# Optimization experiments

Measured on AMD Instinct MI355X. Metric: run time of the kernel, lower is better.

The kernel has to match this reference:

```python
import jax, jax.numpy as jnp
import numpy as np

N_HEADS = 16
KEY_DIM = 64
VAL_DIM = 64
HIDDEN = 1024
SCALE = 1.0 / float(KEY_DIM) ** 0.5


def setup_inputs() -> dict:
    key = jax.random.key(0)
    ks = jax.random.split(key, 16)
    B, Lq, Lk, R = 2, 2048, 2048, 2048
    inp = {
        "query": jax.random.normal(ks[0], (B, Lq, HIDDEN), jnp.float32),
        "value": jax.random.normal(ks[1], (B, Lk, HIDDEN), jnp.float32),
        "positional_embedding": jax.random.normal(ks[2], (R, HIDDEN), jnp.float32),
        "u_weight": jax.random.normal(ks[3], (N_HEADS, KEY_DIM), jnp.float32) * 0.02,
        "v_weight": jax.random.normal(ks[4], (N_HEADS, KEY_DIM), jnp.float32) * 0.02,
        "indices": jax.random.randint(ks[5], (2, Lq, Lk), 0, R, jnp.int64 if jax.config.jax_enable_x64 else jnp.int32),
        "lower": jax.random.uniform(ks[6], (Lq, Lk), jnp.float32),
    }
    s = 0.02
    inp["Wq"] = jax.random.normal(ks[7], (HIDDEN, N_HEADS * KEY_DIM), jnp.float32) * s
    inp["bq"] = jnp.zeros((N_HEADS * KEY_DIM,), jnp.float32)
    inp["Wk"] = jax.random.normal(ks[8], (HIDDEN, N_HEADS * KEY_DIM), jnp.float32) * s
    inp["bk"] = jnp.zeros((N_HEADS * KEY_DIM,), jnp.float32)
    inp["Wv"] = jax.random.normal(ks[9], (HIDDEN, N_HEADS * VAL_DIM), jnp.float32) * s
    inp["bv"] = jnp.zeros((N_HEADS * VAL_DIM,), jnp.float32)
    inp["Wr"] = jax.random.normal(ks[10], (HIDDEN, N_HEADS * KEY_DIM), jnp.float32) * s
    inp["br"] = jnp.zeros((N_HEADS * KEY_DIM,), jnp.float32)
    inp["Wo"] = jax.random.normal(ks[11], (N_HEADS * VAL_DIM, HIDDEN), jnp.float32) * s
    inp["bo"] = jnp.zeros((HIDDEN,), jnp.float32)
    return inp


def reference(query, value, positional_embedding, u_weight, v_weight, indices, lower,
              Wq, bq, Wk, bk, Wv, bv, Wr, br, Wo, bo):
    B, Lq, _ = query.shape
    Lk = value.shape[1]
    R = positional_embedding.shape[0]
    # projections (torch Linear with weights stored as [in, out])
    q = (query @ Wq + bq).reshape(B, Lq, N_HEADS, KEY_DIM)
    k = (value @ Wk + bk).reshape(B, Lk, N_HEADS, KEY_DIM)
    v = (value @ Wv + bv).reshape(B, Lk, N_HEADS, VAL_DIM)
    r = (positional_embedding @ Wr + br).reshape(R, N_HEADS, KEY_DIM)
    # content (AC) and position (BD) score terms -> [i, j, b, n]
    AC = jnp.einsum("bind,bjnd->ijbn", q + u_weight, k)
    BD = jnp.einsum("bind,jnd->ijbn", q + v_weight, r)
    # rel-shift: gather [Lq, R] -> [Lq, Lk] positions, then apply lower mask
    BD = BD[indices[0], indices[1]] * lower[:, :, None, None]
    attn = jax.nn.softmax((AC + BD) * SCALE, axis=1)  # softmax over key dim j
    out = jnp.einsum("ijbn,bjnd->bind", attn, v).reshape(B, Lq, N_HEADS * VAL_DIM)
    return out @ Wo + bo
```

## Files before the change

### kernel.cpp

```cpp
#include <hip/hip_runtime.h>
#include <stdint.h>

typedef __attribute__((ext_vector_type(8))) short short8;
typedef __attribute__((ext_vector_type(4))) float f32x4;
typedef unsigned short u16;
typedef unsigned int u32;
typedef unsigned long long u64;

#define LQ 2048
#define LK 2048
#define RDIM 2048
#define HID 1024
#define NH 16
#define DH 64
#define S2SCALE 0.1803368801111204f

__device__ __forceinline__ float bf2f(u16 u){
  union { unsigned int i; float f; } v; v.i = ((unsigned int)u) << 16; return v.f;
}
__device__ __forceinline__ u16 f2bf(float f){
  union { float f; unsigned int i; } v; v.f = f;
  unsigned int r = v.i + 0x7fffu + ((v.i >> 16) & 1u);
  return (u16)(r >> 16);
}
__device__ __forceinline__ f32x4 fzero(){ f32x4 z = {0.0f, 0.0f, 0.0f, 0.0f}; return z; }

__global__ void k_detect(const u32* __restrict__ q, const u32* __restrict__ idxw,
                         int* __restrict__ flags){
  int t = threadIdx.x;
  u32 w = q[t];
  int b = (w >> 7) & 0xFF;
  unsigned long long mb = __ballot(b >= 100 && b <= 140);
  u32 hi = idxw[2 * t + 1];
  unsigned long long mi = __ballot(hi == 0u);
  if (t == 0){
    flags[0] = (__popcll(mb) >= 48) ? 1 : 0;
    flags[1] = (__popcll(mi) == 64) ? 1 : 0;
  }
}

struct Seg { const void* src; u16* dst; int n4; };
struct SegPack { Seg s[8]; };
__global__ void k_ingestN(SegPack p, const int* __restrict__ flags){
  int f = flags[0];
  Seg sg = p.s[blockIdx.y];
  int stride = gridDim.x * blockDim.x;
  for (int i = blockIdx.x * blockDim.x + threadIdx.x; i < sg.n4; i += stride){
    if (f){
      reinterpret_cast<uint2*>(sg.dst)[i] = reinterpret_cast<const uint2*>(sg.src)[i];
    } else {
      float4 v = reinterpret_cast<const float4*>(sg.src)[i];
      union { u16 h[4]; uint2 u; } t;
      t.h[0] = f2bf(v.x); t.h[1] = f2bf(v.y); t.h[2] = f2bf(v.z); t.h[3] = f2bf(v.w);
      reinterpret_cast<uint2*>(sg.dst)[i] = t.u;
    }
  }
}

struct WPack { const void* src[5]; u16* dst[5]; };
__global__ void k_wtrans(WPack p, const int* __restrict__ flags){
  int f = flags[0];
  const void* W = p.src[blockIdx.z];
  u16* Wt = p.dst[blockIdx.z];
  __shared__ u16 t[64][65];
  int tid = threadIdx.x;
  int bx = blockIdx.x, by = blockIdx.y;
#pragma unroll
  for (int it = 0; it < 16; ++it){
    int id = it * 256 + tid;
    int r = id >> 6, c = id & 63;
    size_t so = (size_t)(by * 64 + r) * HID + bx * 64 + c;
    t[r][c] = f ? ((const u16*)W)[so] : f2bf(((const float*)W)[so]);
  }
  __syncthreads();
#pragma unroll
  for (int it = 0; it < 16; ++it){
    int id = it * 256 + tid;
    int r = id >> 6, c = id & 63;
    Wt[(size_t)(bx * 64 + r) * HID + by * 64 + c] = t[c][r];
  }
}

__global__ void k_goff(const int* __restrict__ idx, int* __restrict__ goff,
                       const int* __restrict__ flags){
  int i64f = flags[1];
  const size_t N = (size_t)LQ * LK;
  size_t stride = (size_t)gridDim.x * blockDim.x;
  for (size_t t = (size_t)blockIdx.x * blockDim.x + threadIdx.x; t < N; t += stride){
    long long a0, a1;
    if (i64f){
      const long long* ip = (const long long*)idx;
      a0 = ip[t]; a1 = ip[N + t];
    } else {
      a0 = idx[t]; a1 = idx[N + t];
    }
    goff[t] = (int)(a0 * RDIM + a1);
  }
}

__global__ void k_gemm(const u16* __restrict__ A, const u16* __restrict__ Bt,
                       const u16* __restrict__ bias,
                       const u16* __restrict__ add0, const u16* __restrict__ add1,
                       void* __restrict__ D0, u16* __restrict__ D1,
                       int headmajor, const int* __restrict__ oflags){
  __shared__ u16 As[128][72];
  __shared__ u16 Bs[128][72];
  int tid = threadIdx.x;
  int l = tid & 63, w = tid >> 6;
  int lr = l & 15, g = l >> 4;
  int wr = w >> 1, wc = w & 1;
  int outf32 = oflags ? (oflags[0] == 0) : 0;
  f32x4 acc[4][4];
#pragma unroll
  for (int a = 0; a < 4; ++a)
#pragma unroll
    for (int bq_ = 0; bq_ < 4; ++bq_) acc[a][bq_] = fzero();
  const size_t arowg = (size_t)blockIdx.x * 128;
  const size_t browg = (size_t)blockIdx.y * 128;
  for (int kt = 0; kt < HID; kt += 64){
#pragma unroll
    for (int it = 0; it < 4; ++it){
      int id = it * 256 + tid;
      int r = id >> 3, ch = id & 7;
      uint4 va = *reinterpret_cast<const uint4*>(A + (arowg + r) * HID + kt + ch * 8);
      *reinterpret_cast<uint4*>(&As[r][ch * 8]) = va;
      uint4 vb = *reinterpret_cast<const uint4*>(Bt + (browg + r) * HID + kt + ch * 8);
      *reinterpret_cast<uint4*>(&Bs[r][ch * 8]) = vb;
    }
    __syncthreads();
#pragma unroll
    for (int ks = 0; ks < 2; ++ks){
      short8 af[4], bfv[4];
#pragma unroll
      for (int mf = 0; mf < 4; ++mf)
        af[mf] = *reinterpret_cast<const short8*>(&As[wr * 64 + mf * 16 + lr][ks * 32 + 8 * g]);
#pragma unroll
      for (int nf = 0; nf < 4; ++nf)
        bfv[nf] = *reinterpret_cast<const short8*>(&Bs[wc * 64 + nf * 16 + lr][ks * 32 + 8 * g]);
#pragma unroll
      for (int mf = 0; mf < 4; ++mf)
#pragma unroll
        for (int nf = 0; nf < 4; ++nf)
          acc[mf][nf] = __builtin_amdgcn_mfma_f32_16x16x32_bf16(af[mf], bfv[nf], acc[mf][nf], 0, 0, 0);
    }
    __syncthreads();
  }
#pragma unroll
  for (int mf = 0; mf < 4; ++mf)
#pragma unroll
    for (int nf = 0; nf < 4; ++nf){
      int col = (int)browg + wc * 64 + nf * 16 + lr;
      float bcol = bf2f(bias[col]);
      float a0 = add0 ? bf2f(add0[col]) : 0.0f;
      float a1 = add1 ? bf2f(add1[col]) : 0.0f;
#pragma unroll
      for (int reg = 0; reg < 4; ++reg){
        int row = (int)arowg + wr * 64 + mf * 16 + 4 * g + reg;
        float base = acc[mf][nf][reg] + bcol;
        if (headmajor == 2){
          int b = row >> 11, i = row & 2047;
          int n32 = col >> 6, d = col & 63;
          u16* Dx = (n32 < NH) ? (u16*)D0 : D1;
          size_t dst = ((size_t)(b * NH + (n32 & (NH - 1))) * LQ + i) * DH + d;
          Dx[dst] = f2bf(base);
        } else if (headmajor == 1){
          int b = row >> 11, i = row & 2047;
          int n = col >> 6, d = col & 63;
          size_t dst = ((size_t)(b * NH + n) * LQ + i) * DH + d;
          ((u16*)D0)[dst] = f2bf(base + a0);
          if (D1) D1[dst] = f2bf(base + a1);
        } else {
          size_t dst = (size_t)row * HID + col;
          if (outf32) ((float*)D0)[dst] = base;
          else        ((u16*)D0)[dst] = f2bf(base);
        }
      }
    }
}

__global__ void k_bdfull16(const u16* __restrict__ qv, const u16* __restrict__ rr,
                           u16* __restrict__ bdf, int bnBase){
  __shared__ u16 tile[32][64][16];
  int tid = threadIdx.x;
  int l = tid & 63, w = tid >> 6;
  int lr = l & 15, g = l >> 4;
  int i0 = blockIdx.x * 32, j0 = blockIdx.y * 64;
#pragma unroll
  for (int hh = 0; hh < 4; ++hh){
    int g_ = w * 4 + hh;
    int bn = bnBase + g_;
    int b = bn >> 4, n = bn & 15;
    const u16* qb = qv + ((size_t)(b * NH + n) * LQ + i0) * DH;
    const u16* rb = rr + ((size_t)n * RDIM + j0) * DH;
    short8 af[2][2];
#pragma unroll
    for (int mf = 0; mf < 2; ++mf)
#pragma unroll
      for (int ks = 0; ks < 2; ++ks)
        af[mf][ks] = *reinterpret_cast<const short8*>(qb + (size_t)(mf * 16 + lr) * DH + ks * 32 + 8 * g);
    f32x4 acc[2][4];
#pragma unroll
    for (int mf = 0; mf < 2; ++mf)
#pragma unroll
      for (int nf = 0; nf < 4; ++nf) acc[mf][nf] = fzero();
#pragma unroll
    for (int nf = 0; nf < 4; ++nf){
#pragma unroll
      for (int ks = 0; ks < 2; ++ks){
        short8 bb = *reinterpret_cast<const short8*>(rb + (size_t)(nf * 16 + lr) * DH + ks * 32 + 8 * g);
#pragma unroll
        for (int mf = 0; mf < 2; ++mf)
          acc[mf][nf] = __builtin_amdgcn_mfma_f32_16x16x32_bf16(af[mf][ks], bb, acc[mf][nf], 0, 0, 0);
      }
    }
#pragma unroll
    for (int mf = 0; mf < 2; ++mf)
#pragma unroll
      for (int nf = 0; nf < 4; ++nf)
#pragma unroll
        for (int reg = 0; reg < 4; ++reg)
          tile[mf * 16 + 4 * g + reg][nf * 16 + lr][g_] = f2bf(acc[mf][nf][reg]);
  }
  __syncthreads();
#pragma unroll
  for (int e = 0; e < 32; ++e){
    int id = e * 256 + tid;
    int line = id >> 2, part = id & 3;
    int ii = line >> 6, jj = line & 63;
    u64 v = *reinterpret_cast<const u64*>(&tile[ii][jj][part * 4]);
    *reinterpret_cast<u64*>(
        bdf + ((size_t)(i0 + ii) * RDIM + (size_t)(j0 + jj)) * 16 + part * 4) = v;
  }
}

template<int G>
__global__ void k_bdfull(const u16* __restrict__ qv, const u16* __restrict__ rr,
                         u16* __restrict__ bdf, int bnBase){
  __shared__ u16 tile[16][32][G];
  int tid = threadIdx.x;
  int l = tid & 63, w = tid >> 6;
  int lr = l & 15, g = l >> 4;
  int i0 = blockIdx.x * 16, j0 = blockIdx.y * 32;
  constexpr int C = (G >= 4) ? (G / 4) : 1;
  if (G >= 4 || w < G){
#pragma unroll
    for (int bi = 0; bi < C; ++bi){
      int g_ = w * C + bi;
      int bn = bnBase + g_;
      int b = bn >> 4, n = bn & 15;
      const u16* qb = qv + ((size_t)(b * NH + n) * LQ + i0) * DH;
      const u16* rb = rr + ((size_t)n * RDIM + j0) * DH;
      f32x4 acc2[2];
      acc2[0] = fzero(); acc2[1] = fzero();
#pragma unroll
      for (int ks = 0; ks < 2; ++ks){
        short8 a = *reinterpret_cast<const short8*>(qb + (size_t)lr * DH + ks * 32 + 8 * g);
#pragma unroll
        for (int nf = 0; nf < 2; ++nf){
          short8 bb = *reinterpret_cast<const short8*>(rb + (size_t)(lr + 16 * nf) * DH + ks * 32 + 8 * g);
          acc2[nf] = __builtin_amdgcn_mfma_f32_16x16x32_bf16(a, bb, acc2[nf], 0, 0, 0);
        }
      }
#pragma unroll
      for (int nf = 0; nf < 2; ++nf){
        int jj = lr + 16 * nf;
#pragma unroll
        for (int reg = 0; reg < 4; ++reg)
          tile[4 * g + reg][jj][g_] = f2bf(acc2[nf][reg]);
      }
    }
  }
  __syncthreads();
  constexpr int W = (G >= 4) ? 4 : G;
  constexpr int PARTS = G / W;
  constexpr int CHUNKS = 512 * PARTS;
#pragma unroll
  for (int e = 0; e < (CHUNKS + 255) / 256; ++e){
    int id = e * 256 + tid;
    if (CHUNKS < 256 * ((CHUNKS + 255) / 256) && id >= CHUNKS) break;
    int line = id / PARTS, part = id % PARTS;
    int ii = line >> 5, jj = line & 31;
    int k = part * W;
    const u16* src = &tile[ii][jj][k];
    u16* dst = bdf + ((size_t)(i0 + ii) * RDIM + (size_t)(j0 + jj)) * G + k;
    if (W == 4)
      *reinterpret_cast<u64*>(dst) = *reinterpret_cast<const u64*>(src);
    else if (W == 2)
      *reinterpret_cast<u32*>(dst) = *reinterpret_cast<const u32*>(src);
    else
      *dst = *src;
  }
}

template<int G>
__global__ void k_gather(const u16* __restrict__ bdf, const int* __restrict__ goff,
                         const u16* __restrict__ lower, u16* __restrict__ bdg){
  __shared__ u16 tile[G][16][32];
  int tid = threadIdx.x;
  int i0 = blockIdx.x * 16, j0 = blockIdx.y * 32;
#pragma unroll
  for (int it = 0; it < 2; ++it){
    int p = it * 256 + tid;
    int ii = p >> 5, jj = p & 31;
    size_t off = (size_t)(i0 + ii) * LK + (j0 + jj);
    int go = goff[off];
    float lw = bf2f(lower[off]);
    const u16* src = bdf + (size_t)go * G;
    union { uint4 q[2]; u32 w2[8]; u16 h[16]; } uv;
    if (G == 16){
      uv.q[0] = *reinterpret_cast<const uint4*>(src);
      uv.q[1] = *reinterpret_cast<const uint4*>(src + 8);
    } else if (G == 8){
      uv.q[0] = *reinterpret_cast<const uint4*>(src);
    } else if (G == 2){
      uv.w2[0] = *reinterpret_cast<const u32*>(src);
    } else {
      uv.h[0] = *src;
    }
#pragma unroll
    for (int k = 0; k < G; ++k)
      tile[k][ii][jj] = f2bf(bf2f(uv.h[k]) * lw);
  }
  __syncthreads();
  constexpr int CHUNKS = G * 128;
#pragma unroll
  for (int e = 0; e < (CHUNKS + 255) / 256; ++e){
    int id = e * 256 + tid;
    if (CHUNKS < 256 * ((CHUNKS + 255) / 256) && id >= CHUNKS) break;
    int g_ = id >> 7, rem = id & 127;
    int ii = rem >> 3, part = rem & 7;
    u64 v = *reinterpret_cast<const u64*>(&tile[g_][ii][part * 4]);
    *reinterpret_cast<u64*>(
        bdg + (size_t)g_ * LQ * LK + (size_t)(i0 + ii) * LK + j0 + part * 4) = v;
  }
}

__global__ void k_flash(const u16* __restrict__ qu, const u16* __restrict__ kk,
                        const u16* __restrict__ vv, const u16* __restrict__ bdg,
                        u16* __restrict__ oo, int bnBase){
  __shared__ u16 klds[128][72];
  __shared__ u16 vtlds[64][136];
  __shared__ u16 plds[4][16][136];
  int tid = threadIdx.x;
  int l = tid & 63, w = tid >> 6;
  int lr = l & 15, g = l >> 4;
  int gi = blockIdx.x;
  int bn = bnBase + gi;
  int b = bn >> 4, n = bn & 15;
  int i0 = blockIdx.y * 64;
  const u16* qb = qu + ((size_t)bn * LQ + i0 + w * 16) * DH;
  short8 aq0 = *reinterpret_cast<const short8*>(qb + (size_t)lr * DH + 8 * g);
  short8 aq1 = *reinterpret_cast<const short8*>(qb + (size_t)lr * DH + 32 + 8 * g);
  f32x4 O[4];
#pragma unroll
  for (int nf = 0; nf < 4; ++nf) O[nf] = fzero();
  float mrun[4], lacc[4];
#pragma unroll
  for (int r = 0; r < 4; ++r){ mrun[r] = -1e30f; lacc[r] = 0.0f; }
  const u16* kbase = kk + (size_t)bn * LK * DH;
  const u16* vbase = vv + (size_t)bn * LK * DH;
  const u16* bdb = bdg + (size_t)gi * LQ * LK + (size_t)(i0 + w * 16) * LK;

  for (int j0 = 0; j0 < LK; j0 += 128){
#pragma unroll
    for (int it = 0; it < 4; ++it){
      int id = it * 256 + tid;
      int r = id >> 3, ch = id & 7;
      uint4 kv = *reinterpret_cast<const uint4*>(kbase + (size_t)(j0 + r) * DH + ch * 8);
      *reinterpret_cast<uint4*>(&klds[r][ch * 8]) = kv;
      uint4 vv4 = *reinterpret_cast<const uint4*>(vbase + (size_t)(j0 + r) * DH + ch * 8);
      u16 tmp[8];
      *reinterpret_cast<uint4*>(tmp) = vv4;
#pragma unroll
      for (int e2 = 0; e2 < 8; ++e2) vtlds[ch * 8 + e2][r] = tmp[e2];
    }
    __syncthreads();

    float sv[8][4];
#pragma unroll
    for (int nf = 0; nf < 8; ++nf){
      f32x4 z = fzero();
      short8 bk0 = *reinterpret_cast<const short8*>(&klds[lr + 16 * nf][8 * g]);
      short8 bk1 = *reinterpret_cast<const short8*>(&klds[lr + 16 * nf][32 + 8 * g]);
      z = __builtin_amdgcn_mfma_f32_16x16x32_bf16(aq0, bk0, z, 0, 0, 0);
      z = __builtin_amdgcn_mfma_f32_16x16x32_bf16(aq1, bk1, z, 0, 0, 0);
#pragma unroll
      for (int reg = 0; reg < 4; ++reg){
        float bd = bf2f(bdb[(size_t)(4 * g + reg) * LK + j0 + lr + 16 * nf]);
        sv[nf][reg] = (z[reg] + bd) * S2SCALE;
      }
    }
    float fs[4];
#pragma unroll
    for (int reg = 0; reg < 4; ++reg){
      float mx = sv[0][reg];
#pragma unroll
      for (int nf = 1; nf < 8; ++nf) mx = fmaxf(mx, sv[nf][reg]);
#pragma unroll
      for (int d = 1; d < 16; d <<= 1) mx = fmaxf(mx, __shfl_xor(mx, d));
      float mnew = fmaxf(mrun[reg], mx);
      fs[reg] = exp2f(mrun[reg] - mnew);
      mrun[reg] = mnew;
      float sumloc = 0.0f;
#pragma unroll
      for (int nf = 0; nf < 8; ++nf){
        sv[nf][reg] = exp2f(sv[nf][reg] - mnew);
        sumloc += sv[nf][reg];
      }
      lacc[reg] = lacc[reg] * fs[reg] + sumloc;
    }
#pragma unroll
    for (int nf = 0; nf < 4; ++nf)
#pragma unroll
      for (int reg = 0; reg < 4; ++reg)
        O[nf][reg] *= fs[reg];
#pragma unroll
    for (int nf = 0; nf < 8; ++nf)
#pragma unroll
      for (int reg = 0; reg < 4; ++reg)
        plds[w][4 * g + reg][lr + 16 * nf] = f2bf(sv[nf][reg]);
    short8 pa[4];
#pragma unroll
    for (int ks = 0; ks < 4; ++ks)
      pa[ks] = *reinterpret_cast<const short8*>(&plds[w][lr][ks * 32 + 8 * g]);
#pragma unroll
    for (int nf = 0; nf < 4; ++nf){
#pragma unroll
      for (int ks = 0; ks < 4; ++ks){
        short8 bv = *reinterpret_cast<const short8*>(&vtlds[lr + 16 * nf][ks * 32 + 8 * g]);
        O[nf] = __builtin_amdgcn_mfma_f32_16x16x32_bf16(pa[ks], bv, O[nf], 0, 0, 0);
      }
    }
    __syncthreads();
  }
  float lsum[4];
#pragma unroll
  for (int reg = 0; reg < 4; ++reg){
    float s = lacc[reg];
#pragma unroll
    for (int d = 1; d < 16; d <<= 1) s += __shfl_xor(s, d);
    lsum[reg] = s;
  }
#pragma unroll
  for (int nf = 0; nf < 4; ++nf)
#pragma unroll
    for (int reg = 0; reg < 4; ++reg){
      int i = i0 + w * 16 + 4 * g + reg;
      float vo = O[nf][reg] / lsum[reg];
      oo[((size_t)(b * LQ + i)) * HID + n * DH + lr + 16 * nf] = f2bf(vo);
    }
}

extern "C" void kernel_launch(void* const* d_in, const int* in_sizes, int n_in,
                              void* d_out, int out_size, void* d_ws, size_t ws_size,
                              hipStream_t stream){
  const void* query = d_in[0];
  const void* value = d_in[1];
  const void* pos   = d_in[2];
  const void* uw    = d_in[3];
  const void* vw    = d_in[4];
  const int* idx    = (const int*)d_in[5];
  const void* lower = d_in[6];
  const void* Wq = d_in[7];  const void* bq = d_in[8];
  const void* Wk = d_in[9];  const void* bk = d_in[10];
  const void* Wv = d_in[11]; const void* bv = d_in[12];
  const void* Wr = d_in[13]; const void* br = d_in[14];
  const void* Wo = d_in[15]; const void* bo = d_in[16];
  (void)in_sizes; (void)n_in; (void)out_size;

  char* ws = (char*)d_ws;
  const size_t MB = (size_t)1 << 20;
  u16* cquery = (u16*)(ws + 0 * MB);
  u16* cvalue = (u16*)(ws + 8 * MB);
  int* goff   = (int*)(ws + 0 * MB);
  u16* cpos   = (u16*)(ws + 16 * MB);
  u16* clower = (u16*)(ws + 20 * MB);
  char* sm = ws + 38 * MB;
  u16* cuw = (u16*)(sm + 0 * 4096);
  u16* cvw = (u16*)(sm + 1 * 4096);
  u16* cbq = (u16*)(sm + 2 * 4096);
  u16* cbk = (u16*)(sm + 3 * 4096);
  u16* cbv = cbk + 1024;
  u16* cbr = (u16*)(sm + 5 * 4096);
  u16* cbo = (u16*)(sm + 6 * 4096);
  int* flags = (int*)(sm + 7 * 4096);
  u16* wqt = (u16*)(ws + 39 * MB);
  u16* wkt = (u16*)(ws + 41 * MB);
  u16* wvt = (u16*)(ws + 43 * MB);
  u16* wrt = (u16*)(ws + 45 * MB);
  u16* wot = (u16*)(ws + 47 * MB);
  u16* qu  = (u16*)(ws + 49 * MB);
  u16* qv  = (u16*)(ws + 57 * MB);
  u16* kkp = (u16*)(ws + 65 * MB);
  u16* vvp = (u16*)(ws + 73 * MB);
  u16* rrp = (u16*)(ws + 81 * MB);
  u16* oo  = (u16*)(ws + 85 * MB);
  u16* bdf = (u16*)(ws + 96 * MB);

  int G = 1;
  if (ws_size >= 352 * MB) G = 16;
  else if (ws_size >= 224 * MB) G = 8;
  else if (ws_size >= 128 * MB) G = 2;
  u16* bdg = (u16*)(ws + (96 + 8 * (size_t)G) * MB);

  dim3 blk(256);
  k_detect<<<1, 64, 0, stream>>>((const u32*)query, (const u32*)idx, flags);

  {
    SegPack big;
    big.s[0] = { query, cquery, 2 * LQ * HID / 4 };
    big.s[1] = { value, cvalue, 2 * LK * HID / 4 };
    big.s[2] = { pos,   cpos,   RDIM * HID / 4 };
    big.s[3] = { lower, clower, LQ * LK / 4 };
    for (int i = 4; i < 8; ++i) big.s[i] = { nullptr, nullptr, 0 };
    k_ingestN<<<dim3(512, 4), blk, 0, stream>>>(big, flags);
    SegPack sml;
    sml.s[0] = { uw, cuw, NH * DH / 4 };
    sml.s[1] = { vw, cvw, NH * DH / 4 };
    sml.s[2] = { bq, cbq, HID / 4 };
    sml.s[3] = { bk, cbk, HID / 4 };
    sml.s[4] = { bv, cbv, HID / 4 };
    sml.s[5] = { br, cbr, HID / 4 };
    sml.s[6] = { bo, cbo, HID / 4 };
    sml.s[7] = { nullptr, nullptr, 0 };
    k_ingestN<<<dim3(4, 7), blk, 0, stream>>>(sml, flags);
  }
  {
    WPack wp;
    wp.src[0] = Wq; wp.dst[0] = wqt;
    wp.src[1] = Wk; wp.dst[1] = wkt;
    wp.src[2] = Wv; wp.dst[2] = wvt;
    wp.src[3] = Wr; wp.dst[3] = wrt;
    wp.src[4] = Wo; wp.dst[4] = wot;
    k_wtrans<<<dim3(16, 16, 5), blk, 0, stream>>>(wp, flags);
  }

  k_gemm<<<dim3(32, 8), blk, 0, stream>>>(cquery, wqt, cbq, cuw, cvw, qu, qv, 1, nullptr);
  k_gemm<<<dim3(32, 16), blk, 0, stream>>>(cvalue, wkt, cbk, nullptr, nullptr, kkp, vvp, 2, nullptr);
  k_gemm<<<dim3(16, 8), blk, 0, stream>>>(cpos, wrt, cbr, nullptr, nullptr, rrp, nullptr, 1, nullptr);

  k_goff<<<dim3(1024), blk, 0, stream>>>(idx, goff, flags);

  for (int b0 = 0; b0 < 2 * NH; b0 += G){
    if (G == 16){
      k_bdfull16<<<dim3(64, 32), blk, 0, stream>>>(qv, rrp, bdf, b0);
      k_gather<16><<<dim3(128, 64), blk, 0, stream>>>(bdf, goff, clower, bdg);
    } else if (G == 8){
      k_bdfull<8><<<dim3(128, 64), blk, 0, stream>>>(qv, rrp, bdf, b0);
      k_gather<8><<<dim3(128, 64), blk, 0, stream>>>(bdf, goff, clower, bdg);
    } else if (G == 2){
      k_bdfull<2><<<dim3(128, 64), blk, 0, stream>>>(qv, rrp, bdf, b0);
      k_gather<2><<<dim3(128, 64), blk, 0, stream>>>(bdf, goff, clower, bdg);
    } else {
      k_bdfull<1><<<dim3(128, 64), blk, 0, stream>>>(qv, rrp, bdf, b0);
      k_gather<1><<<dim3(128, 64), blk, 0, stream>>>(bdf, goff, clower, bdg);
    }
    k_flash<<<dim3(G, 32), blk, 0, stream>>>(qu, kkp, vvp, bdg, oo, b0);
  }
  k_gemm<<<dim3(32, 8), blk, 0, stream>>>(oo, wot, cbo, nullptr, nullptr, d_out, nullptr, 0, flags);
}
```

Measured before the change: 989.3 us.

## Stage BD tile through swizzled LDS and swizzle V-transpose layout

```diff
diff --git a/kernel.cpp b/kernel.cpp
--- a/kernel.cpp
+++ b/kernel.cpp
@@ -330,8 +330,8 @@
     int g_ = id >> 7, rem = id & 127;
     int ii = rem >> 3, part = rem & 7;
     u64 v = *reinterpret_cast<const u64*>(&tile[g_][ii][part * 4]);
-    *reinterpret_cast<u64*>(
-        bdg + (size_t)g_ * LQ * LK + (size_t)(i0 + ii) * LK + j0 + part * 4) = v;
+    __builtin_nontemporal_store(v, reinterpret_cast<u64*>(
+        bdg + (size_t)g_ * LQ * LK + (size_t)(i0 + ii) * LK + j0 + part * 4));
   }
 }
 
@@ -339,8 +339,8 @@
                         const u16* __restrict__ vv, const u16* __restrict__ bdg,
                         u16* __restrict__ oo, int bnBase){
   __shared__ u16 klds[128][72];
-  __shared__ u16 vtlds[64][136];
-  __shared__ u16 plds[4][16][136];
+  __shared__ u16 vtlds[64][128];
+  __shared__ u16 scr[64][136];
   int tid = threadIdx.x;
   int l = tid & 63, w = tid >> 6;
   int lr = l & 15, g = l >> 4;
@@ -359,7 +359,7 @@
   for (int r = 0; r < 4; ++r){ mrun[r] = -1e30f; lacc[r] = 0.0f; }
   const u16* kbase = kk + (size_t)bn * LK * DH;
   const u16* vbase = vv + (size_t)bn * LK * DH;
-  const u16* bdb = bdg + (size_t)gi * LQ * LK + (size_t)(i0 + w * 16) * LK;
+  const u16* bdb = bdg + (size_t)gi * LQ * LK + (size_t)i0 * LK;
 
   for (int j0 = 0; j0 < LK; j0 += 128){
 #pragma unroll
@@ -371,8 +371,21 @@
       uint4 vv4 = *reinterpret_cast<const uint4*>(vbase + (size_t)(j0 + r) * DH + ch * 8);
       u16 tmp[8];
       *reinterpret_cast<uint4*>(tmp) = vv4;
-#pragma unroll
-      for (int e2 = 0; e2 < 8; ++e2) vtlds[ch * 8 + e2][r] = tmp[e2];
+      int cb = ((r >> 3) ^ ch) * 8 + (r & 7);
+#pragma unroll
+      for (int e2 = 0; e2 < 8; ++e2) vtlds[ch * 8 + e2][cb] = tmp[e2];
+    }
+#pragma unroll
+    for (int it = 0; it < 4; ++it){
+      int id = it * 256 + tid;
+      int row = id >> 4, ch = id & 15;
+      const u16* src = bdb + (size_t)row * LK + j0 + ch * 8;
+      u64 lo = __builtin_nontemporal_load(reinterpret_cast<const u64*>(src));
+      u64 hi = __builtin_nontemporal_load(reinterpret_cast<const u64*>(src + 4));
+      int cc = ch ^ (row & 7);
+      u16* dst = &scr[row][cc * 8];
+      *reinterpret_cast<u64*>(dst) = lo;
+      *reinterpret_cast<u64*>(dst + 4) = hi;
     }
     __syncthreads();
 
@@ -384,9 +397,12 @@
       short8 bk1 = *reinterpret_cast<const short8*>(&klds[lr + 16 * nf][32 + 8 * g]);
       z = __builtin_amdgcn_mfma_f32_16x16x32_bf16(aq0, bk0, z, 0, 0, 0);
       z = __builtin_amdgcn_mfma_f32_16x16x32_bf16(aq1, bk1, z, 0, 0, 0);
+      int col = lr + 16 * nf;
 #pragma unroll
       for (int reg = 0; reg < 4; ++reg){
-        float bd = bf2f(bdb[(size_t)(4 * g + reg) * LK + j0 + lr + 16 * nf]);
+        int prow = w * 16 + 4 * g + reg;
+        int cc = (col >> 3) ^ (prow & 7);
+        float bd = bf2f(scr[prow][cc * 8 + (col & 7)]);
         sv[nf][reg] = (z[reg] + bd) * S2SCALE;
       }
     }
@@ -415,19 +431,28 @@
       for (int reg = 0; reg < 4; ++reg)
         O[nf][reg] *= fs[reg];
 #pragma unroll
-    for (int nf = 0; nf < 8; ++nf)
-#pragma unroll
-      for (int reg = 0; reg < 4; ++reg)
-        plds[w][4 * g + reg][lr + 16 * nf] = f2bf(sv[nf][reg]);
+    for (int nf = 0; nf < 8; ++nf){
+      int col = lr + 16 * nf;
+#pragma unroll
+      for (int reg = 0; reg < 4; ++reg){
+        int prow = w * 16 + 4 * g + reg;
+        int cc = (col >> 3) ^ (prow & 7);
+        scr[prow][cc * 8 + (col & 7)] = f2bf(sv[nf][reg]);
+      }
+    }
     short8 pa[4];
 #pragma unroll
-    for (int ks = 0; ks < 4; ++ks)
-      pa[ks] = *reinterpret_cast<const short8*>(&plds[w][lr][ks * 32 + 8 * g]);
+    for (int ks = 0; ks < 4; ++ks){
+      int cc = (ks * 4 + g) ^ (lr & 7);
+      pa[ks] = *reinterpret_cast<const short8*>(&scr[w * 16 + lr][cc * 8]);
+    }
 #pragma unroll
     for (int nf = 0; nf < 4; ++nf){
+      int d = lr + 16 * nf;
 #pragma unroll
       for (int ks = 0; ks < 4; ++ks){
-        short8 bv = *reinterpret_cast<const short8*>(&vtlds[lr + 16 * nf][ks * 32 + 8 * g]);
+        int cv = (ks * 4 + g) ^ ((d >> 3) & 7);
+        short8 bv = *reinterpret_cast<const short8*>(&vtlds[d][cv * 8]);
         O[nf] = __builtin_amdgcn_mfma_f32_16x16x32_bf16(pa[ks], bv, O[nf], 0, 0, 0);
       }
     }
```

After: 1.429 ms. 44.4% more time.

## Double-buffer K/V and BD loads in flash kernel, split BD gather into 8-head halves

Applied to the files above, without the earlier changes.

```diff
diff --git a/kernel.cpp b/kernel.cpp
--- a/kernel.cpp
+++ b/kernel.cpp
@@ -178,16 +178,16 @@
     }
 }
 
-__global__ void k_bdfull16(const u16* __restrict__ qv, const u16* __restrict__ rr,
-                           u16* __restrict__ bdf, int bnBase){
-  __shared__ u16 tile[32][64][16];
+__global__ void k_bdfull8(const u16* __restrict__ qv, const u16* __restrict__ rr,
+                          u16* __restrict__ bdf, int bnBase){
+  __shared__ u16 tile[32][64][8];
   int tid = threadIdx.x;
   int l = tid & 63, w = tid >> 6;
   int lr = l & 15, g = l >> 4;
   int i0 = blockIdx.x * 32, j0 = blockIdx.y * 64;
 #pragma unroll
-  for (int hh = 0; hh < 4; ++hh){
-    int g_ = w * 4 + hh;
+  for (int hh = 0; hh < 2; ++hh){
+    int g_ = w * 2 + hh;
     int bn = bnBase + g_;
     int b = bn >> 4, n = bn & 15;
     const u16* qb = qv + ((size_t)(b * NH + n) * LQ + i0) * DH;
@@ -223,13 +223,13 @@
   }
   __syncthreads();
 #pragma unroll
-  for (int e = 0; e < 32; ++e){
+  for (int e = 0; e < 16; ++e){
     int id = e * 256 + tid;
-    int line = id >> 2, part = id & 3;
+    int line = id >> 1, part = id & 1;
     int ii = line >> 6, jj = line & 63;
     u64 v = *reinterpret_cast<const u64*>(&tile[ii][jj][part * 4]);
     *reinterpret_cast<u64*>(
-        bdf + ((size_t)(i0 + ii) * RDIM + (size_t)(j0 + jj)) * 16 + part * 4) = v;
+        bdf + ((size_t)(i0 + ii) * RDIM + (size_t)(j0 + jj)) * 8 + part * 4) = v;
   }
 }
 
@@ -241,54 +241,40 @@
   int l = tid & 63, w = tid >> 6;
   int lr = l & 15, g = l >> 4;
   int i0 = blockIdx.x * 16, j0 = blockIdx.y * 32;
-  constexpr int C = (G >= 4) ? (G / 4) : 1;
-  if (G >= 4 || w < G){
-#pragma unroll
-    for (int bi = 0; bi < C; ++bi){
-      int g_ = w * C + bi;
-      int bn = bnBase + g_;
-      int b = bn >> 4, n = bn & 15;
-      const u16* qb = qv + ((size_t)(b * NH + n) * LQ + i0) * DH;
-      const u16* rb = rr + ((size_t)n * RDIM + j0) * DH;
-      f32x4 acc2[2];
-      acc2[0] = fzero(); acc2[1] = fzero();
-#pragma unroll
-      for (int ks = 0; ks < 2; ++ks){
-        short8 a = *reinterpret_cast<const short8*>(qb + (size_t)lr * DH + ks * 32 + 8 * g);
-#pragma unroll
-        for (int nf = 0; nf < 2; ++nf){
-          short8 bb = *reinterpret_cast<const short8*>(rb + (size_t)(lr + 16 * nf) * DH + ks * 32 + 8 * g);
-          acc2[nf] = __builtin_amdgcn_mfma_f32_16x16x32_bf16(a, bb, acc2[nf], 0, 0, 0);
-        }
+  if (w < G){
+    int g_ = w;
+    int bn = bnBase + g_;
+    int b = bn >> 4, n = bn & 15;
+    const u16* qb = qv + ((size_t)(b * NH + n) * LQ + i0) * DH;
+    const u16* rb = rr + ((size_t)n * RDIM + j0) * DH;
+    f32x4 acc2[2];
+    acc2[0] = fzero(); acc2[1] = fzero();
+#pragma unroll
+    for (int ks = 0; ks < 2; ++ks){
+      short8 a = *reinterpret_cast<const short8*>(qb + (size_t)lr * DH + ks * 32 + 8 * g);
+#pragma unroll
+      for (int nf = 0; nf < 2; ++nf){
+        short8 bb = *reinterpret_cast<const short8*>(rb + (size_t)(lr + 16 * nf) * DH + ks * 32 + 8 * g);
+        acc2[nf] = __builtin_amdgcn_mfma_f32_16x16x32_bf16(a, bb, acc2[nf], 0, 0, 0);
       }
-#pragma unroll
-      for (int nf = 0; nf < 2; ++nf){
-        int jj = lr + 16 * nf;
-#pragma unroll
-        for (int reg = 0; reg < 4; ++reg)
-          tile[4 * g + reg][jj][g_] = f2bf(acc2[nf][reg]);
-      }
+    }
+#pragma unroll
+    for (int nf = 0; nf < 2; ++nf){
+      int jj = lr + 16 * nf;
+#pragma unroll
+      for (int reg = 0; reg < 4; ++reg)
+        tile[4 * g + reg][jj][g_] = f2bf(acc2[nf][reg]);
     }
   }
   __syncthreads();
-  constexpr int W = (G >= 4) ? 4 : G;
-  constexpr int PARTS = G / W;
-  constexpr int CHUNKS = 512 * PARTS;
-#pragma unroll
-  for (int e = 0; e < (CHUNKS + 255) / 256; ++e){
+  constexpr int CHUNKS = 512;
+#pragma unroll
+  for (int e = 0; e < (CHUNKS * G + 255) / 256 && e * 256 < CHUNKS * G; ++e){
     int id = e * 256 + tid;
-    if (CHUNKS < 256 * ((CHUNKS + 255) / 256) && id >= CHUNKS) break;
-    int line = id / PARTS, part = id % PARTS;
+    if (id >= CHUNKS * G) break;
+    int line = id / G, k = id % G;
     int ii = line >> 5, jj = line & 31;
-    int k = part * W;
-    const u16* src = &tile[ii][jj][k];
-    u16* dst = bdf + ((size_t)(i0 + ii) * RDIM + (size_t)(j0 + jj)) * G + k;
-    if (W == 4)
-      *reinterpret_cast<u64*>(dst) = *reinterpret_cast<const u64*>(src);
-    else if (W == 2)
-      *reinterpret_cast<u32*>(dst) = *reinterpret_cast<const u32*>(src);
-    else
-      *dst = *src;
+    bdf[((size_t)(i0 + ii) * RDIM + (size_t)(j0 + jj)) * G + k] = tile[ii][jj][k];
   }
 }
 
@@ -330,16 +316,79 @@
     int g_ = id >> 7, rem = id & 127;
     int ii = rem >> 3, part = rem & 7;
     u64 v = *reinterpret_cast<const u64*>(&tile[g_][ii][part * 4]);
-    *reinterpret_cast<u64*>(
-        bdg + (size_t)g_ * LQ * LK + (size_t)(i0 + ii) * LK + j0 + part * 4) = v;
-  }
-}
-
-__global__ void k_flash(const u16* __restrict__ qu, const u16* __restrict__ kk,
-                        const u16* __restrict__ vv, const u16* __restrict__ bdg,
-                        u16* __restrict__ oo, int bnBase){
+    __builtin_nontemporal_store(v, reinterpret_cast<u64*>(
+        bdg + (size_t)g_ * LQ * LK + (size_t)(i0 + ii) * LK + j0 + part * 4));
+  }
+}
+
+__device__ __forceinline__ void flash_compute(
+    const u16 (&bd)[8][4], int lr, int g,
+    const short8& aq0, const short8& aq1,
+    f32x4* O, float* mrun, float* lacc,
+    u16 (*klds)[72], u16 (*vtlds)[128], u16 (*pldsw)[136]){
+  float sv[8][4];
+#pragma unroll
+  for (int nf = 0; nf < 8; ++nf){
+    f32x4 z = fzero();
+    short8 bk0 = *reinterpret_cast<const short8*>(&klds[lr + 16 * nf][8 * g]);
+    short8 bk1 = *reinterpret_cast<const short8*>(&klds[lr + 16 * nf][32 + 8 * g]);
+    z = __builtin_amdgcn_mfma_f32_16x16x32_bf16(aq0, bk0, z, 0, 0, 0);
+    z = __builtin_amdgcn_mfma_f32_16x16x32_bf16(aq1, bk1, z, 0, 0, 0);
+#pragma unroll
+    for (int reg = 0; reg < 4; ++reg)
+      sv[nf][reg] = (z[reg] + bf2f(bd[nf][reg])) * S2SCALE;
+  }
+  float fs[4];
+#pragma unroll
+  for (int reg = 0; reg < 4; ++reg){
+    float mx = sv[0][reg];
+#pragma unroll
+    for (int nf = 1; nf < 8; ++nf) mx = fmaxf(mx, sv[nf][reg]);
+#pragma unroll
+    for (int d = 1; d < 16; d <<= 1) mx = fmaxf(mx, __shfl_xor(mx, d));
+    float mnew = fmaxf(mrun[reg], mx);
+    fs[reg] = exp2f(mrun[reg] - mnew);
+    mrun[reg] = mnew;
+    float sumloc = 0.0f;
+#pragma unroll
+    for (int nf = 0; nf < 8; ++nf){
+      sv[nf][reg] = exp2f(sv[nf][reg] - mnew);
+      sumloc += sv[nf][reg];
+    }
+    lacc[reg] = lacc[reg] * fs[reg] + sumloc;
+  }
+#pragma unroll
+  for (int nf = 0; nf < 4; ++nf)
+#pragma unroll
+    for (int reg = 0; reg < 4; ++reg)
+      O[nf][reg] *= fs[reg];
+#pragma unroll
+  for (int nf = 0; nf < 8; ++nf)
+#pragma unroll
+    for (int reg = 0; reg < 4; ++reg)
+      pldsw[4 * g + reg][lr + 16 * nf] = f2bf(sv[nf][reg]);
+  short8 pa[4];
+#pragma unroll
+  for (int ks = 0; ks < 4; ++ks)
+    pa[ks] = *reinterpret_cast<const short8*>(&pldsw[lr][ks * 32 + 8 * g]);
+#pragma unroll
+  for (int nf = 0; nf < 4; ++nf){
+    int d = lr + 16 * nf;
+#pragma unroll
+    for (int ks = 0; ks < 4; ++ks){
+      int cv = ((ks * 4 + g) ^ (d >> 3)) * 8;
+      short8 bv = *reinterpret_cast<const short8*>(&vtlds[d][cv]);
+      O[nf] = __builtin_amdgcn_mfma_f32_16x16x32_bf16(pa[ks], bv, O[nf], 0, 0, 0);
+    }
+  }
+}
+
+__global__ __launch_bounds__(256) void k_flash(
+    const u16* __restrict__ qu, const u16* __restrict__ kk,
+    const u16* __restrict__ vv, const u16* __restrict__ bdg,
+    u16* __restrict__ oo, int bnBase){
   __shared__ u16 klds[128][72];
-  __shared__ u16 vtlds[64][136];
+  __shared__ u16 vtlds[64][128];
   __shared__ u16 plds[4][16][136];
   int tid = threadIdx.x;
   int l = tid & 63, w = tid >> 6;
@@ -359,80 +408,51 @@
   for (int r = 0; r < 4; ++r){ mrun[r] = -1e30f; lacc[r] = 0.0f; }
   const u16* kbase = kk + (size_t)bn * LK * DH;
   const u16* vbase = vv + (size_t)bn * LK * DH;
-  const u16* bdb = bdg + (size_t)gi * LQ * LK + (size_t)(i0 + w * 16) * LK;
-
-  for (int j0 = 0; j0 < LK; j0 += 128){
-#pragma unroll
-    for (int it = 0; it < 4; ++it){
-      int id = it * 256 + tid;
-      int r = id >> 3, ch = id & 7;
-      uint4 kv = *reinterpret_cast<const uint4*>(kbase + (size_t)(j0 + r) * DH + ch * 8);
-      *reinterpret_cast<uint4*>(&klds[r][ch * 8]) = kv;
-      uint4 vv4 = *reinterpret_cast<const uint4*>(vbase + (size_t)(j0 + r) * DH + ch * 8);
-      u16 tmp[8];
-      *reinterpret_cast<uint4*>(tmp) = vv4;
-#pragma unroll
-      for (int e2 = 0; e2 < 8; ++e2) vtlds[ch * 8 + e2][r] = tmp[e2];
-    }
+  const u16* bdw = bdg + (size_t)gi * LQ * LK + (size_t)(i0 + w * 16) * LK;
+  u16 (*pldsw)[136] = plds[w];
+
+  uint4 kv[8];
+  u16 bdA[8][4], bdB[8][4];
+
+#define LOADKV(J_) do { _Pragma("unroll") for (int it_ = 0; it_ < 4; ++it_){ \
+    int id_ = it_ * 256 + tid; int r_ = id_ >> 3, ch_ = id_ & 7; \
+    kv[it_]     = *reinterpret_cast<const uint4*>(kbase + (size_t)((J_) + r_) * DH + ch_ * 8); \
+    kv[4 + it_] = *reinterpret_cast<const uint4*>(vbase + (size_t)((J_) + r_) * DH + ch_ * 8); } } while(0)
+
+#define WRITELDS() do { _Pragma("unroll") for (int it_ = 0; it_ < 4; ++it_){ \
+    int id_ = it_ * 256 + tid; int r_ = id_ >> 3, ch_ = id_ & 7; \
+    *reinterpret_cast<uint4*>(&klds[r_][ch_ * 8]) = kv[it_]; \
+    u16 tmp_[8]; *reinterpret_cast<uint4*>(tmp_) = kv[4 + it_]; \
+    int cb_ = r_ ^ (ch_ * 8); \
+    _Pragma("unroll") for (int e_ = 0; e_ < 8; ++e_) vtlds[ch_ * 8 + e_][cb_] = tmp_[e_]; } } while(0)
+
+#define LOADBD(B_, J_) do { _Pragma("unroll") for (int nf_ = 0; nf_ < 8; ++nf_) \
+    { _Pragma("unroll") for (int rg_ = 0; rg_ < 4; ++rg_) \
+      B_[nf_][rg_] = bdw[(size_t)(4 * g + rg_) * LK + (J_) + lr + 16 * nf_]; } } while(0)
+
+  LOADKV(0); LOADBD(bdA, 0);
+  WRITELDS();
+  __syncthreads();
+
+  for (int tp = 0; tp < 8; ++tp){
+    int jA = tp * 256, jB = jA + 128;
+    LOADKV(jB); LOADBD(bdB, jB);
+    flash_compute(bdA, lr, g, aq0, aq1, O, mrun, lacc, klds, vtlds, pldsw);
     __syncthreads();
-
-    float sv[8][4];
-#pragma unroll
-    for (int nf = 0; nf < 8; ++nf){
-      f32x4 z = fzero();
-      short8 bk0 = *reinterpret_cast<const short8*>(&klds[lr + 16 * nf][8 * g]);
-      short8 bk1 = *reinterpret_cast<const short8*>(&klds[lr + 16 * nf][32 + 8 * g]);
-      z = __builtin_amdgcn_mfma_f32_16x16x32_bf16(aq0, bk0, z, 0, 0, 0);
-      z = __builtin_amdgcn_mfma_f32_16x16x32_bf16(aq1, bk1, z, 0, 0, 0);
-#pragma unroll
-      for (int reg = 0; reg < 4; ++reg){
-        float bd = bf2f(bdb[(size_t)(4 * g + reg) * LK + j0 + lr + 16 * nf]);
-        sv[nf][reg] = (z[reg] + bd) * S2SCALE;
-      }
-    }
-    float fs[4];
-#pragma unroll
-    for (int reg = 0; reg < 4; ++reg){
-      float mx = sv[0][reg];
-#pragma unroll
-      for (int nf = 1; nf < 8; ++nf) mx = fmaxf(mx, sv[nf][reg]);
-#pragma unroll
-      for (int d = 1; d < 16; d <<= 1) mx = fmaxf(mx, __shfl_xor(mx, d));
-      float mnew = fmaxf(mrun[reg], mx);
-      fs[reg] = exp2f(mrun[reg] - mnew);
-      mrun[reg] = mnew;
-      float sumloc = 0.0f;
-#pragma unroll
-      for (int nf = 0; nf < 8; ++nf){
-        sv[nf][reg] = exp2f(sv[nf][reg] - mnew);
-        sumloc += sv[nf][reg];
-      }
-      lacc[reg] = lacc[reg] * fs[reg] + sumloc;
-    }
-#pragma unroll
-    for (int nf = 0; nf < 4; ++nf)
-#pragma unroll
-      for (int reg = 0; reg < 4; ++reg)
-        O[nf][reg] *= fs[reg];
-#pragma unroll
-    for (int nf = 0; nf < 8; ++nf)
-#pragma unroll
-      for (int reg = 0; reg < 4; ++reg)
-        plds[w][4 * g + reg][lr + 16 * nf] = f2bf(sv[nf][reg]);
-    short8 pa[4];
-#pragma unroll
-    for (int ks = 0; ks < 4; ++ks)
-      pa[ks] = *reinterpret_cast<const short8*>(&plds[w][lr][ks * 32 + 8 * g]);
-#pragma unroll
-    for (int nf = 0; nf < 4; ++nf){
-#pragma unroll
-      for (int ks = 0; ks < 4; ++ks){
-        short8 bv = *reinterpret_cast<const short8*>(&vtlds[lr + 16 * nf][ks * 32 + 8 * g]);
-        O[nf] = __builtin_amdgcn_mfma_f32_16x16x32_bf16(pa[ks], bv, O[nf], 0, 0, 0);
-      }
-    }
+    WRITELDS();
     __syncthreads();
-  }
+    if (tp < 7){ LOADKV(jA + 256); LOADBD(bdA, jA + 256); }
+    flash_compute(bdB, lr, g, aq0, aq1, O, mrun, lacc, klds, vtlds, pldsw);
+    if (tp < 7){
+      __syncthreads();
+      WRITELDS();
+      __syncthreads();
+    }
+  }
+#undef LOADKV
+#undef WRITELDS
+#undef LOADBD
+
   float lsum[4];
 #pragma unroll
   for (int reg = 0; reg < 4; ++reg){
@@ -497,12 +517,6 @@
   u16* oo  = (u16*)(ws + 85 * MB);
   u16* bdf = (u16*)(ws + 96 * MB);
 
-  int G = 1;
-  if (ws_size >= 352 * MB) G = 16;
-  else if (ws_size >= 224 * MB) G = 8;
-  else if (ws_size >= 128 * MB) G = 2;
-  u16* bdg = (u16*)(ws + (96 + 8 * (size_t)G) * MB);
-
   dim3 blk(256);
   k_detect<<<1, 64, 0, stream>>>((const u32*)query, (const u32*)idx, flags);
 
@@ -541,21 +555,36 @@
 
   k_goff<<<dim3(1024), blk, 0, stream>>>(idx, goff, flags);
 
-  for (int b0 = 0; b0 < 2 * NH; b0 += G){
-    if (G == 16){
-      k_bdfull16<<<dim3(64, 32), blk, 0, stream>>>(qv, rrp, bdf, b0);
-      k_gather<16><<<dim3(128, 64), blk, 0, stream>>>(bdf, goff, clower, bdg);
-    } else if (G == 8){
-      k_bdfull<8><<<dim3(128, 64), blk, 0, stream>>>(qv, rrp, bdf, b0);
+  if (ws_size >= 288 * MB){
+    u16* bdg = (u16*)(ws + 160 * MB);
+    for (int b0 = 0; b0 < 2 * NH; b0 += 16){
+      k_bdfull8<<<dim3(64, 32), blk, 0, stream>>>(qv, rrp, bdf, b0);
       k_gather<8><<<dim3(128, 64), blk, 0, stream>>>(bdf, goff, clower, bdg);
-    } else if (G == 2){
+      k_bdfull8<<<dim3(64, 32), blk, 0, stream>>>(qv, rrp, bdf, b0 + 8);
+      k_gather<8><<<dim3(128, 64), blk, 0, stream>>>(bdf, goff, clower, bdg + (size_t)8 * LQ * LK);
+      k_flash<<<dim3(16, 32), blk, 0, stream>>>(qu, kkp, vvp, bdg, oo, b0);
+    }
+  } else if (ws_size >= 224 * MB){
+    u16* bdg = (u16*)(ws + 160 * MB);
+    for (int b0 = 0; b0 < 2 * NH; b0 += 8){
+      k_bdfull8<<<dim3(64, 32), blk, 0, stream>>>(qv, rrp, bdf, b0);
+      k_gather<8><<<dim3(128, 64), blk, 0, stream>>>(bdf, goff, clower, bdg);
+      k_flash<<<dim3(8, 32), blk, 0, stream>>>(qu, kkp, vvp, bdg, oo, b0);
+    }
+  } else if (ws_size >= 128 * MB){
+    u16* bdg = (u16*)(ws + 112 * MB);
+    for (int b0 = 0; b0 < 2 * NH; b0 += 2){
       k_bdfull<2><<<dim3(128, 64), blk, 0, stream>>>(qv, rrp, bdf, b0);
       k_gather<2><<<dim3(128, 64), blk, 0, stream>>>(bdf, goff, clower, bdg);
-    } else {
+      k_flash<<<dim3(2, 32), blk, 0, stream>>>(qu, kkp, vvp, bdg, oo, b0);
+    }
+  } else {
+    u16* bdg = (u16*)(ws + 104 * MB);
+    for (int b0 = 0; b0 < 2 * NH; b0 += 1){
       k_bdfull<1><<<dim3(128, 64), blk, 0, stream>>>(qv, rrp, bdf, b0);
       k_gather<1><<<dim3(128, 64), blk, 0, stream>>>(bdf, goff, clower, bdg);
-    }
-    k_flash<<<dim3(G, 32), blk, 0, stream>>>(qu, kkp, vvp, bdg, oo, b0);
+      k_flash<<<dim3(1, 32), blk, 0, stream>>>(qu, kkp, vvp, bdg, oo, b0);
+    }
   }
   k_gemm<<<dim3(32, 8), blk, 0, stream>>>(oo, wot, cbo, nullptr, nullptr, d_out, nullptr, 0, flags);
 }
```

New measurement: 957.7 us. 3.2% less time.
